# Kernel optimization log

Hardware: AMD Instinct MI355X
Metric: run time of the kernel (lower is better)

The kernel has to match this reference:

```python
import jax, jax.numpy as jnp
import numpy as np

DIM = 1024
HEADS = 16
HEAD_DIM = 64
INNER = HEADS * HEAD_DIM
SCALE = HEAD_DIM ** -0.5


def setup_inputs() -> dict:
    key = jax.random.key(0)
    k1, k2, k3, k4 = jax.random.split(key, 4)
    x = jax.random.normal(k1, (4, 2048, DIM), dtype=jnp.float32)
    # nn.Linear(dim, 3*inner) without bias; weight stored [out, in], we keep [in, out]
    w_qkv = jax.random.normal(k2, (DIM, 3 * INNER), dtype=jnp.float32) * (DIM ** -0.5)
    w_proj = jax.random.normal(k3, (INNER, DIM), dtype=jnp.float32) * (INNER ** -0.5)
    b_proj = jax.random.normal(k4, (DIM,), dtype=jnp.float32) * 0.01
    return {"x": x, "w_qkv": w_qkv, "w_proj": w_proj, "b_proj": b_proj}


def reference(x, w_qkv, w_proj, b_proj):
    B, N, _ = x.shape
    qkv = x @ w_qkv                                   # [B,N,3*inner]
    qkv = qkv.reshape(B, N, 3, HEADS, HEAD_DIM)
    q = qkv[:, :, 0].transpose(0, 2, 1, 3)           # [B,H,N,D]
    k = qkv[:, :, 1].transpose(0, 2, 1, 3)
    v = qkv[:, :, 2].transpose(0, 2, 1, 3)
    attn = jnp.einsum("bhqd,bhkd->bhqk", q, k) * SCALE
    attn = jax.nn.softmax(attn, axis=-1)
    out = jnp.einsum("bhqk,bhkd->bhqd", attn, v)     # [B,H,N,D]
    out = out.transpose(0, 2, 1, 3).reshape(B, N, INNER)
    return out @ w_proj + b_proj
```

## Files before the change

### kernel.cpp

```cpp
#include <hip/hip_runtime.h>

typedef unsigned short u16;
typedef unsigned int   u32;
typedef __attribute__((ext_vector_type(2))) float    f32x2;
typedef __attribute__((ext_vector_type(4))) float    f32x4;
typedef __attribute__((ext_vector_type(8))) __bf16   bf16x8;
typedef __attribute__((ext_vector_type(8))) unsigned short u16x8;
typedef __attribute__((ext_vector_type(4))) unsigned short u16x4;
typedef __attribute__((ext_vector_type(4))) float    float4v;

#define MFMA16(a,b,c) __builtin_amdgcn_mfma_f32_16x16x32_bf16((a),(b),(c),0,0,0)
#define QSCALE 0.18033688011112042f

__device__ __forceinline__ u16 f2b(float f){
  union { float f; unsigned u; } v; v.f = f;
  return (u16)((v.u + 0x7fffu + ((v.u >> 16) & 1u)) >> 16);
}

__device__ __forceinline__ u32 cvt_pk_bf16(float lo, float hi){
  u32 r;
  asm("v_cvt_pk_bf16_f32 %0, %1, %2" : "=v"(r) : "v"(lo), "v"(hi));
  return r;
}

__device__ __forceinline__ float exp2_raw(float x){
  float r;
  asm("v_exp_f32 %0, %1" : "=v"(r) : "v"(x));
  return r;
}

__device__ __forceinline__ f32x2 lo2(f32x4 v){ return __builtin_shufflevector(v, v, 0, 1); }
__device__ __forceinline__ f32x2 hi2(f32x4 v){ return __builtin_shufflevector(v, v, 2, 3); }
__device__ __forceinline__ f32x2 pkmax(f32x2 a, f32x2 b){ return __builtin_elementwise_max(a, b); }

__device__ __forceinline__ void gload_lds16(const void* g, void* l){
  __builtin_amdgcn_global_load_lds(
      (const __attribute__((address_space(1))) void*)g,
      (__attribute__((address_space(3))) void*)l, 16, 0, 0);
}

__global__ void cast_f32_bf16(const float* __restrict__ in, u16* __restrict__ out, int n4){
  int i = blockIdx.x * blockDim.x + threadIdx.x;
  int st = gridDim.x * blockDim.x;
  for (; i < n4; i += st){
    float4v v = ((const float4v*)in)[i];
    u16x4 o;
    o[0] = f2b(v[0]); o[1] = f2b(v[1]); o[2] = f2b(v[2]); o[3] = f2b(v[3]);
    ((u16x4*)out)[i] = o;
  }
}

__global__ void tcast(const float* __restrict__ src, u16* __restrict__ dst, int R, int C){
  __shared__ float tile[32][33];
  int tx = threadIdx.x, ty = threadIdx.y;
  int c0 = blockIdx.x * 32, r0 = blockIdx.y * 32;
  #pragma unroll
  for (int i = 0; i < 4; i++)
    tile[ty + i*8][tx] = src[(long)(r0 + ty + i*8) * C + c0 + tx];
  __syncthreads();
  #pragma unroll
  for (int i = 0; i < 4; i++)
    dst[(long)(c0 + ty + i*8) * R + r0 + tx] = f2b(tile[tx][ty + i*8]);
}

template<int MODE>
__global__ __launch_bounds__(256, 2) void gemm_bt(
    const u16* __restrict__ A, const u16* __restrict__ Bt,
    int M, int N, int K,
    float* __restrict__ outF, const float* __restrict__ bias,
    u16* __restrict__ qb, u16* __restrict__ kb, u16* __restrict__ vtb)
{
  __shared__ u16 a_lds[128*32];
  __shared__ u16 b_lds[128*32];
  const int t  = threadIdx.x;
  const int l  = t & 63;
  const int w  = t >> 6;
  const int wm = w >> 1, wn = w & 1;
  const int lr = l & 15, lg = l >> 4;
  const long mbase = (long)blockIdx.x * 128;
  const long nbase = (long)blockIdx.y * 128;

  f32x4 z = {0.f, 0.f, 0.f, 0.f};
  f32x4 acc[4][4];
  #pragma unroll
  for (int i = 0; i < 4; i++)
    #pragma unroll
    for (int j = 0; j < 4; j++) acc[i][j] = z;

  const int sr = t >> 2;
  const int sc = (t & 3) * 8;
  const u16* Ab = A  + mbase * K;
  const u16* Bb = Bt + nbase * K;

  for (int k0 = 0; k0 < K; k0 += 32){
    __syncthreads();
    gload_lds16(Ab + (long)sr      * K + k0 + sc, &a_lds[t*8]);
    gload_lds16(Ab + (long)(sr+64) * K + k0 + sc, &a_lds[2048 + t*8]);
    gload_lds16(Bb + (long)sr      * K + k0 + sc, &b_lds[t*8]);
    gload_lds16(Bb + (long)(sr+64) * K + k0 + sc, &b_lds[2048 + t*8]);
    __syncthreads();

    bf16x8 af[4], bfr[4];
    #pragma unroll
    for (int i = 0; i < 4; i++)
      af[i] = *(const bf16x8*)&a_lds[(wm*64 + i*16 + lr)*32 + lg*8];
    #pragma unroll
    for (int j = 0; j < 4; j++)
      bfr[j] = *(const bf16x8*)&b_lds[(wn*64 + j*16 + lr)*32 + lg*8];
    #pragma unroll
    for (int i = 0; i < 4; i++)
      #pragma unroll
      for (int j = 0; j < 4; j++)
        acc[i][j] = MFMA16(af[i], bfr[j], acc[i][j]);
  }

  if (MODE == 0){
    #pragma unroll
    for (int i = 0; i < 4; i++){
      #pragma unroll
      for (int j = 0; j < 4; j++){
        int col   = (int)nbase + wn*64 + j*16 + lr;
        int which = col >> 10;
        int h     = (col >> 6) & 15;
        int d     = col & 63;
        int m0    = (int)mbase + wm*64 + i*16 + lg*4;
        int b     = m0 >> 11, ns0 = m0 & 2047;
        int bh    = (b << 4) + h;
        if (which == 2){
          u16x4 pk;
          #pragma unroll
          for (int r = 0; r < 4; r++) pk[r] = f2b(acc[i][j][r]);
          *(u16x4*)&vtb[((long)bh*64 + d)*2048 + ns0] = pk;
        } else {
          u16* dst  = (which == 0) ? qb : kb;
          float scl = (which == 0) ? QSCALE : 1.0f;
          #pragma unroll
          for (int r = 0; r < 4; r++)
            dst[((long)bh * 2048 + ns0 + r) * 64 + d] = f2b(acc[i][j][r] * scl);
        }
      }
    }
  } else {
    #pragma unroll
    for (int i = 0; i < 4; i++){
      #pragma unroll
      for (int j = 0; j < 4; j++){
        int c = (int)nbase + wn*64 + j*16 + lr;
        float bv = bias[c];
        #pragma unroll
        for (int r = 0; r < 4; r++){
          int m = (int)mbase + wm*64 + i*16 + lg*4 + r;
          outF[(long)m * N + c] = acc[i][j][r] + bv;
        }
      }
    }
  }
}

__global__ __launch_bounds__(256, 2) void attn_fused(
    const u16* __restrict__ qb, const u16* __restrict__ kb,
    const u16* __restrict__ vtb, u16* __restrict__ ob)
{
  __shared__ u16 k_lds[2][64*64];
  __shared__ u16 vt_lds[2][64*64];
  const int t  = threadIdx.x;
  const int l  = t & 63, lr = l & 15, lg = l >> 4;
  const int w  = t >> 6;
  const int bid = blockIdx.x;
  const int vid = (bid & 7) * 128 + (bid >> 3);
  const int bh = vid >> 4, qt = vid & 15;
  const int qrow = qt*128 + w*32;
  const int h7 = lr & 7;

  const u16* Qp = qb + ((long)bh*2048 + qrow)*64;
  bf16x8 qfA0 = *(const bf16x8*)&Qp[lr*64 + lg*8];
  bf16x8 qfA1 = *(const bf16x8*)&Qp[lr*64 + 32 + lg*8];
  bf16x8 qfB0 = *(const bf16x8*)&Qp[(16+lr)*64 + lg*8];
  bf16x8 qfB1 = *(const bf16x8*)&Qp[(16+lr)*64 + 32 + lg*8];

  const int r1 = t >> 3;
  const int cx = ((t & 7) ^ (r1 & 7)) * 8;
  const u16* Kp = kb  + (long)bh*2048*64;
  const u16* Vt = vtb + (long)bh*64*2048;
  const int koff0 = r1*64 + cx,        koff1 = (r1+32)*64 + cx;
  const int voff0 = r1*2048 + cx,      voff1 = (r1+32)*2048 + cx;

#define STAGE(kv, buf) do { \
    gload_lds16(Kp + (long)(kv)*64 + koff0, &k_lds[buf][t*8]); \
    gload_lds16(Kp + (long)(kv)*64 + koff1, &k_lds[buf][2048 + t*8]); \
    gload_lds16(Vt + (kv) + voff0, &vt_lds[buf][t*8]); \
    gload_lds16(Vt + (kv) + voff1, &vt_lds[buf][2048 + t*8]); \
  } while(0)

  f32x4 z = {0.f,0.f,0.f,0.f};
  f32x4 oaccA[4] = {z,z,z,z}, oaccB[4] = {z,z,z,z};
  float mrunA = -1e30f, lrunA = 0.f;
  float mrunB = -1e30f, lrunB = 0.f;

  STAGE(0, 0);
  for (int it = 0; it < 32; ++it){
    const int cur = it & 1;
    __syncthreads();
    if (it < 31) STAGE((it+1)*64, cur^1);

    const u16* kl = k_lds[cur];
    const u16* vl = vt_lds[cur];

    f32x4 stA[4], stB[4];
    __builtin_amdgcn_s_setprio(1);
    #pragma unroll
    for (int k4 = 0; k4 < 4; k4++){
      const int row = (k4*16 + lr)*64;
      bf16x8 kf0 = *(const bf16x8*)&kl[row + ((0+lg)^h7)*8];
      bf16x8 kf1 = *(const bf16x8*)&kl[row + ((4+lg)^h7)*8];
      stA[k4] = MFMA16(kf0, qfA0, z);
      stA[k4] = MFMA16(kf1, qfA1, stA[k4]);
      stB[k4] = MFMA16(kf0, qfB0, z);
      stB[k4] = MFMA16(kf1, qfB1, stB[k4]);
    }
    __builtin_amdgcn_s_setprio(0);

    f32x2 a0 = pkmax(pkmax(lo2(stA[0]), hi2(stA[0])), pkmax(lo2(stA[1]), hi2(stA[1])));
    f32x2 a1 = pkmax(pkmax(lo2(stA[2]), hi2(stA[2])), pkmax(lo2(stA[3]), hi2(stA[3])));
    a0 = pkmax(a0, a1);
    float mxA = fmaxf(a0[0], a0[1]);
    mxA = fmaxf(mxA, __shfl_xor(mxA, 16, 64));
    mxA = fmaxf(mxA, __shfl_xor(mxA, 32, 64));
    f32x2 b0 = pkmax(pkmax(lo2(stB[0]), hi2(stB[0])), pkmax(lo2(stB[1]), hi2(stB[1])));
    f32x2 b1 = pkmax(pkmax(lo2(stB[2]), hi2(stB[2])), pkmax(lo2(stB[3]), hi2(stB[3])));
    b0 = pkmax(b0, b1);
    float mxB = fmaxf(b0[0], b0[1]);
    mxB = fmaxf(mxB, __shfl_xor(mxB, 16, 64));
    mxB = fmaxf(mxB, __shfl_xor(mxB, 32, 64));

    if (__any((mxA > mrunA + 11.5f) | (mxB > mrunB + 11.5f))){
      float mnA = fmaxf(mrunA, mxA), alA = exp2_raw(mrunA - mnA);
      mrunA = mnA; lrunA *= alA;
      float mnB = fmaxf(mrunB, mxB), alB = exp2_raw(mrunB - mnB);
      mrunB = mnB; lrunB *= alB;
      #pragma unroll
      for (int r = 0; r < 4; r++){
        float arA = __shfl(alA, lg*4 + r, 64);
        float arB = __shfl(alB, lg*4 + r, 64);
        oaccA[0][r] *= arA; oaccA[1][r] *= arA; oaccA[2][r] *= arA; oaccA[3][r] *= arA;
        oaccB[0][r] *= arB; oaccB[1][r] *= arB; oaccB[2][r] *= arB; oaccB[3][r] *= arB;
      }
    }

    u32 wvA[4][2], wvB[4][2];
    f32x2 mA2 = {mrunA, mrunA}, mB2 = {mrunB, mrunB};
    f32x2 sA2 = {0.f, 0.f},    sB2 = {0.f, 0.f};
    #pragma unroll
    for (int k4 = 0; k4 < 4; k4++){
      f32x2 e0 = lo2(stA[k4]) - mA2, e1 = hi2(stA[k4]) - mA2;
      e0[0] = exp2_raw(e0[0]); e0[1] = exp2_raw(e0[1]);
      e1[0] = exp2_raw(e1[0]); e1[1] = exp2_raw(e1[1]);
      sA2 += e0 + e1;
      wvA[k4][0] = cvt_pk_bf16(e0[0], e0[1]);
      wvA[k4][1] = cvt_pk_bf16(e1[0], e1[1]);
      f32x2 f0 = lo2(stB[k4]) - mB2, f1 = hi2(stB[k4]) - mB2;
      f0[0] = exp2_raw(f0[0]); f0[1] = exp2_raw(f0[1]);
      f1[0] = exp2_raw(f1[0]); f1[1] = exp2_raw(f1[1]);
      sB2 += f0 + f1;
      wvB[k4][0] = cvt_pk_bf16(f0[0], f0[1]);
      wvB[k4][1] = cvt_pk_bf16(f1[0], f1[1]);
    }
    float rsA = sA2[0] + sA2[1];
    rsA += __shfl_xor(rsA, 16, 64);
    rsA += __shfl_xor(rsA, 32, 64);
    lrunA += rsA;
    float rsB = sB2[0] + sB2[1];
    rsB += __shfl_xor(rsB, 16, 64);
    rsB += __shfl_xor(rsB, 32, 64);
    lrunB += rsB;

    union { u32 u[4]; bf16x8 v; } paA0, paA1, paB0, paB1;
    paA0.u[0]=wvA[0][0]; paA0.u[1]=wvA[0][1]; paA0.u[2]=wvA[1][0]; paA0.u[3]=wvA[1][1];
    paA1.u[0]=wvA[2][0]; paA1.u[1]=wvA[2][1]; paA1.u[2]=wvA[3][0]; paA1.u[3]=wvA[3][1];
    paB0.u[0]=wvB[0][0]; paB0.u[1]=wvB[0][1]; paB0.u[2]=wvB[1][0]; paB0.u[3]=wvB[1][1];
    paB1.u[0]=wvB[2][0]; paB1.u[1]=wvB[2][1]; paB1.u[2]=wvB[3][0]; paB1.u[3]=wvB[3][1];

    const int vhalf = (lg & 1) * 4;
    const int cA    = lg >> 1;
    #pragma unroll
    for (int nt = 0; nt < 4; nt++){
      const int rb = (nt*16 + lr)*64;
      u16x4 a0_ = *(const u16x4*)&vl[rb + ((cA     ^ h7)*8) + vhalf];
      u16x4 a1_ = *(const u16x4*)&vl[rb + (((cA+2) ^ h7)*8) + vhalf];
      u16x4 a2_ = *(const u16x4*)&vl[rb + (((cA+4) ^ h7)*8) + vhalf];
      u16x4 a3_ = *(const u16x4*)&vl[rb + (((cA+6) ^ h7)*8) + vhalf];
      u16x8 s0 = __builtin_shufflevector(a0_, a1_, 0,1,2,3,4,5,6,7);
      u16x8 s1 = __builtin_shufflevector(a2_, a3_, 0,1,2,3,4,5,6,7);
      __builtin_amdgcn_s_setprio(1);
      oaccA[nt] = MFMA16(paA0.v, *(bf16x8*)&s0, oaccA[nt]);
      oaccA[nt] = MFMA16(paA1.v, *(bf16x8*)&s1, oaccA[nt]);
      oaccB[nt] = MFMA16(paB0.v, *(bf16x8*)&s0, oaccB[nt]);
      oaccB[nt] = MFMA16(paB1.v, *(bf16x8*)&s1, oaccB[nt]);
      __builtin_amdgcn_s_setprio(0);
    }
  }
#undef STAGE

  float linvA = 1.0f / lrunA, linvB = 1.0f / lrunB;
  const int b = bh >> 4, h = bh & 15;
  #pragma unroll
  for (int r = 0; r < 4; r++){
    float lrA = __shfl(linvA, lg*4 + r, 64);
    float lrB = __shfl(linvB, lg*4 + r, 64);
    long mA = (long)b*2048 + qrow + lg*4 + r;
    long mB = mA + 16;
    #pragma unroll
    for (int nt = 0; nt < 4; nt++){
      ob[mA*1024 + h*64 + nt*16 + lr] = f2b(oaccA[nt][r] * lrA);
      ob[mB*1024 + h*64 + nt*16 + lr] = f2b(oaccB[nt][r] * lrB);
    }
  }
}

extern "C" void kernel_launch(void* const* d_in, const int* in_sizes, int n_in,
                              void* d_out, int out_size, void* d_ws, size_t ws_size,
                              hipStream_t stream)
{
  const float* x      = (const float*)d_in[0];
  const float* w_qkv  = (const float*)d_in[1];
  const float* w_proj = (const float*)d_in[2];
  const float* b_proj = (const float*)d_in[3];
  float* out = (float*)d_out;

  char* ws = (char*)d_ws;
  size_t off = 0;
  u16* xb     = (u16*)(ws + off);
  u16* obuf   = xb;
  off += (size_t)8192*1024*2;
  u16* wqkvt  = (u16*)(ws + off); off += (size_t)3072*1024*2;
  u16* wprojt = (u16*)(ws + off); off += (size_t)1024*1024*2;
  u16* qbuf   = (u16*)(ws + off); off += (size_t)64*2048*64*2;
  u16* kbuf   = (u16*)(ws + off); off += (size_t)64*2048*64*2;
  u16* vtb    = (u16*)(ws + off); off += (size_t)64*64*2048*2;

  cast_f32_bf16<<<2048, 256, 0, stream>>>(x, xb, (8192*1024)/4);
  tcast<<<dim3(96, 32), dim3(32, 8), 0, stream>>>(w_qkv, wqkvt, 1024, 3072);
  tcast<<<dim3(32, 32), dim3(32, 8), 0, stream>>>(w_proj, wprojt, 1024, 1024);

  gemm_bt<0><<<dim3(64, 24), 256, 0, stream>>>(xb, wqkvt, 8192, 3072, 1024,
                                               nullptr, nullptr, qbuf, kbuf, vtb);
  attn_fused<<<dim3(1024), 256, 0, stream>>>(qbuf, kbuf, vtb, obuf);
  gemm_bt<1><<<dim3(64, 8), 256, 0, stream>>>(obuf, wprojt, 8192, 1024, 1024,
                                              out, b_proj, nullptr, nullptr, nullptr);
}
```

Baseline: 211.0 us.

## Rewrite GEMMs as 8-wave 256x128 tiles with pipelined swizzled LDS staging

Replaces the 128x128, 4-wave, single-buffered GEMM with a 256x128, 8-wave kernel. It uses double-buffered dynamic LDS with XOR-swizzled layout, K-step 64, and fine-grained staging interleaved with MFMA phases using vmcnt waits, barriers and setprio. This targets global-load latency exposure and LDS bank conflicts in the QKV and projection GEMMs. It adds complexity, uses more LDS (96KB per block, which may limit occupancy), and launches fewer blocks.

```diff
diff --git a/kernel.cpp b/kernel.cpp
--- a/kernel.cpp
+++ b/kernel.cpp
@@ -64,93 +64,172 @@
 }
 
 template<int MODE>
-__global__ __launch_bounds__(256, 2) void gemm_bt(
+__global__ __launch_bounds__(512, 2) void gemm8(
     const u16* __restrict__ A, const u16* __restrict__ Bt,
     int M, int N, int K,
     float* __restrict__ outF, const float* __restrict__ bias,
     u16* __restrict__ qb, u16* __restrict__ kb, u16* __restrict__ vtb)
 {
-  __shared__ u16 a_lds[128*32];
-  __shared__ u16 b_lds[128*32];
+  extern __shared__ u16 lds[];
+  u16* aL = lds;
+  u16* bL = lds + 32768;
+
   const int t  = threadIdx.x;
-  const int l  = t & 63;
+  const int l  = t & 63, lr = l & 15, lg = l >> 4;
   const int w  = t >> 6;
-  const int wm = w >> 1, wn = w & 1;
-  const int lr = l & 15, lg = l >> 4;
-  const long mbase = (long)blockIdx.x * 128;
+  const int wm = w >> 2, wn = w & 3;
+  const long mbase = (long)blockIdx.x * 256;
   const long nbase = (long)blockIdx.y * 128;
 
-  f32x4 z = {0.f, 0.f, 0.f, 0.f};
-  f32x4 acc[4][4];
+  const int xr0 = t >> 3;
+  const int xc  = t & 7;
+  const int xswz = (xc ^ (xr0 & 7)) << 3;
+
+#define STG(F_) do { \
+    const int T_ = (F_) >> 2, h_ = (F_) & 3, buf_ = T_ & 1; \
+    if ((h_ & 1) == 0){ const int ah = h_ >> 1; \
+      const u16* g_ = A + (mbase + ah*128 + xr0)*(long)K + T_*64 + xswz; \
+      u16* d_ = aL + buf_*16384 + ah*8192 + t*8; \
+      gload_lds16(g_, d_); \
+      gload_lds16(g_ + 64*(long)K, d_ + 4096); \
+    } else { const int bh_ = h_ >> 1; \
+      const u16* g_ = Bt + (nbase + bh_*64 + xr0)*(long)K + T_*64 + xswz; \
+      gload_lds16(g_, bL + buf_*8192 + bh_*4096 + t*8); } \
+  } while(0)
+
+#define VMCNT(n) asm volatile("s_waitcnt vmcnt(" #n ")" ::: "memory")
+#define BAR() __builtin_amdgcn_s_barrier()
+
+  f32x4 z = {0.f,0.f,0.f,0.f};
+  f32x4 acc[8][2];
   #pragma unroll
-  for (int i = 0; i < 4; i++)
-    #pragma unroll
-    for (int j = 0; j < 4; j++) acc[i][j] = z;
-
-  const int sr = t >> 2;
-  const int sc = (t & 3) * 8;
-  const u16* Ab = A  + mbase * K;
-  const u16* Bb = Bt + nbase * K;
-
-  for (int k0 = 0; k0 < K; k0 += 32){
-    __syncthreads();
-    gload_lds16(Ab + (long)sr      * K + k0 + sc, &a_lds[t*8]);
-    gload_lds16(Ab + (long)(sr+64) * K + k0 + sc, &a_lds[2048 + t*8]);
-    gload_lds16(Bb + (long)sr      * K + k0 + sc, &b_lds[t*8]);
-    gload_lds16(Bb + (long)(sr+64) * K + k0 + sc, &b_lds[2048 + t*8]);
-    __syncthreads();
-
-    bf16x8 af[4], bfr[4];
-    #pragma unroll
-    for (int i = 0; i < 4; i++)
-      af[i] = *(const bf16x8*)&a_lds[(wm*64 + i*16 + lr)*32 + lg*8];
-    #pragma unroll
-    for (int j = 0; j < 4; j++)
-      bfr[j] = *(const bf16x8*)&b_lds[(wn*64 + j*16 + lr)*32 + lg*8];
-    #pragma unroll
-    for (int i = 0; i < 4; i++)
-      #pragma unroll
-      for (int j = 0; j < 4; j++)
-        acc[i][j] = MFMA16(af[i], bfr[j], acc[i][j]);
+  for (int a = 0; a < 8; a++){ acc[a][0] = z; acc[a][1] = z; }
+
+  STG(0); STG(1); STG(2); STG(3); STG(4);
+  VMCNT(2);
+  BAR();
+
+  for (int T = 0; T < 16; ++T){
+    const int abuf = (T & 1) * 16384;
+    const int bbuf = (T & 1) * 8192;
+    const int F = 4 * T;
+    bf16x8 a0[4][2], a1[4][2], bj0[2], bj1[2];
+
+    #pragma unroll
+    for (int i = 0; i < 4; i++){
+      const int ra = wm*128 + i*16 + lr;
+      #pragma unroll
+      for (int k = 0; k < 2; k++)
+        a0[i][k] = *(const bf16x8*)&aL[abuf + ra*64 + (((k*4+lg)^(ra&7))<<3)];
+    }
+    {
+      const int rb = wn*32 + lr;
+      #pragma unroll
+      for (int k = 0; k < 2; k++)
+        bj0[k] = *(const bf16x8*)&bL[bbuf + rb*64 + (((k*4+lg)^(rb&7))<<3)];
+    }
+    if (F + 5 < 64) STG(F + 5);
+    VMCNT(1);
+    BAR();
+    __builtin_amdgcn_s_setprio(1);
+    #pragma unroll
+    for (int k = 0; k < 2; k++)
+      #pragma unroll
+      for (int i = 0; i < 4; i++)
+        acc[i][0] = MFMA16(a0[i][k], bj0[k], acc[i][0]);
+    __builtin_amdgcn_s_setprio(0);
+    BAR();
+
+    {
+      const int rb = wn*32 + 16 + lr;
+      #pragma unroll
+      for (int k = 0; k < 2; k++)
+        bj1[k] = *(const bf16x8*)&bL[bbuf + rb*64 + (((k*4+lg)^(rb&7))<<3)];
+    }
+    if (F + 6 < 64) STG(F + 6);
+    VMCNT(2);
+    BAR();
+    __builtin_amdgcn_s_setprio(1);
+    #pragma unroll
+    for (int k = 0; k < 2; k++)
+      #pragma unroll
+      for (int i = 0; i < 4; i++)
+        acc[i][1] = MFMA16(a0[i][k], bj1[k], acc[i][1]);
+    __builtin_amdgcn_s_setprio(0);
+    BAR();
+
+    #pragma unroll
+    for (int i = 0; i < 4; i++){
+      const int ra = wm*128 + 64 + i*16 + lr;
+      #pragma unroll
+      for (int k = 0; k < 2; k++)
+        a1[i][k] = *(const bf16x8*)&aL[abuf + ra*64 + (((k*4+lg)^(ra&7))<<3)];
+    }
+    if (F + 7 < 64) STG(F + 7);
+    VMCNT(1);
+    BAR();
+    __builtin_amdgcn_s_setprio(1);
+    #pragma unroll
+    for (int k = 0; k < 2; k++)
+      #pragma unroll
+      for (int i = 0; i < 4; i++)
+        acc[4+i][1] = MFMA16(a1[i][k], bj1[k], acc[4+i][1]);
+    __builtin_amdgcn_s_setprio(0);
+    BAR();
+
+    if (F + 8 < 64) STG(F + 8);
+    if (T < 14) { VMCNT(2); } else { VMCNT(0); }
+    BAR();
+    __builtin_amdgcn_s_setprio(1);
+    #pragma unroll
+    for (int k = 0; k < 2; k++)
+      #pragma unroll
+      for (int i = 0; i < 4; i++)
+        acc[4+i][0] = MFMA16(a1[i][k], bj0[k], acc[4+i][0]);
+    __builtin_amdgcn_s_setprio(0);
+    BAR();
   }
+#undef STG
+#undef VMCNT
+#undef BAR
 
   if (MODE == 0){
     #pragma unroll
-    for (int i = 0; i < 4; i++){
-      #pragma unroll
-      for (int j = 0; j < 4; j++){
-        int col   = (int)nbase + wn*64 + j*16 + lr;
+    for (int a = 0; a < 8; a++){
+      #pragma unroll
+      for (int j = 0; j < 2; j++){
+        int col   = (int)nbase + wn*32 + j*16 + lr;
         int which = col >> 10;
         int h     = (col >> 6) & 15;
         int d     = col & 63;
-        int m0    = (int)mbase + wm*64 + i*16 + lg*4;
+        int m0    = (int)mbase + wm*128 + a*16 + lg*4;
         int b     = m0 >> 11, ns0 = m0 & 2047;
         int bh    = (b << 4) + h;
         if (which == 2){
           u16x4 pk;
           #pragma unroll
-          for (int r = 0; r < 4; r++) pk[r] = f2b(acc[i][j][r]);
+          for (int r = 0; r < 4; r++) pk[r] = f2b(acc[a][j][r]);
           *(u16x4*)&vtb[((long)bh*64 + d)*2048 + ns0] = pk;
         } else {
           u16* dst  = (which == 0) ? qb : kb;
           float scl = (which == 0) ? QSCALE : 1.0f;
           #pragma unroll
           for (int r = 0; r < 4; r++)
-            dst[((long)bh * 2048 + ns0 + r) * 64 + d] = f2b(acc[i][j][r] * scl);
+            dst[((long)bh * 2048 + ns0 + r) * 64 + d] = f2b(acc[a][j][r] * scl);
         }
       }
     }
   } else {
     #pragma unroll
-    for (int i = 0; i < 4; i++){
-      #pragma unroll
-      for (int j = 0; j < 4; j++){
-        int c = (int)nbase + wn*64 + j*16 + lr;
+    for (int a = 0; a < 8; a++){
+      #pragma unroll
+      for (int j = 0; j < 2; j++){
+        int c = (int)nbase + wn*32 + j*16 + lr;
         float bv = bias[c];
         #pragma unroll
         for (int r = 0; r < 4; r++){
-          int m = (int)mbase + wm*64 + i*16 + lg*4 + r;
-          outF[(long)m * N + c] = acc[i][j][r] + bv;
+          int m = (int)mbase + wm*128 + a*16 + lg*4 + r;
+          outF[(long)m * N + c] = acc[a][j][r] + bv;
         }
       }
     }
@@ -338,13 +417,18 @@
   u16* kbuf   = (u16*)(ws + off); off += (size_t)64*2048*64*2;
   u16* vtb    = (u16*)(ws + off); off += (size_t)64*64*2048*2;
 
+  hipFuncSetAttribute(reinterpret_cast<const void*>(&gemm8<0>),
+                      hipFuncAttributeMaxDynamicSharedMemorySize, 98304);
+  hipFuncSetAttribute(reinterpret_cast<const void*>(&gemm8<1>),
+                      hipFuncAttributeMaxDynamicSharedMemorySize, 98304);
+
   cast_f32_bf16<<<2048, 256, 0, stream>>>(x, xb, (8192*1024)/4);
   tcast<<<dim3(96, 32), dim3(32, 8), 0, stream>>>(w_qkv, wqkvt, 1024, 3072);
   tcast<<<dim3(32, 32), dim3(32, 8), 0, stream>>>(w_proj, wprojt, 1024, 1024);
 
-  gemm_bt<0><<<dim3(64, 24), 256, 0, stream>>>(xb, wqkvt, 8192, 3072, 1024,
-                                               nullptr, nullptr, qbuf, kbuf, vtb);
+  gemm8<0><<<dim3(32, 24), 512, 98304, stream>>>(xb, wqkvt, 8192, 3072, 1024,
+                                                 nullptr, nullptr, qbuf, kbuf, vtb);
   attn_fused<<<dim3(1024), 256, 0, stream>>>(qbuf, kbuf, vtb, obuf);
-  gemm_bt<1><<<dim3(64, 8), 256, 0, stream>>>(obuf, wprojt, 8192, 1024, 1024,
-                                              out, b_proj, nullptr, nullptr, nullptr);
-}
+  gemm8<1><<<dim3(32, 8), 512, 98304, stream>>>(obuf, wprojt, 8192, 1024, 1024,
+                                                out, b_proj, nullptr, nullptr, nullptr);
+}
```

New measurement: 210.4 us. Within noise of the previous version (-0.3%).
